# Performance work log

Hardware: AMD Instinct MI355X
Metric: run time of the kernel (lower is better)

## Reference

```python
import jax, jax.numpy as jnp
import numpy as np

N_NODES = 50000
N_EDGES = 800000


def setup_inputs() -> dict:
    key = jax.random.key(0)
    ks = jax.random.split(key, 8)
    return {
        "x": jax.random.normal(ks[0], (N_NODES, 256), dtype=jnp.float32),
        "adj_vals": jax.random.uniform(ks[1], (N_EDGES,), dtype=jnp.float32),
        "rows": jax.random.randint(ks[2], (N_EDGES,), 0, N_NODES, dtype=jnp.int32),
        "cols": jax.random.randint(ks[3], (N_EDGES,), 0, N_NODES, dtype=jnp.int32),
        "W1": jax.random.normal(ks[4], (256, 256), dtype=jnp.float32) * (1.0 / np.sqrt(256)),
        "b1": jnp.zeros((256,), dtype=jnp.float32),
        "W2": jax.random.normal(ks[5], (256, 256), dtype=jnp.float32) * (1.0 / np.sqrt(256)),
        "b2": jnp.zeros((256,), dtype=jnp.float32),
        "W3": jax.random.normal(ks[6], (256, 128), dtype=jnp.float32) * (1.0 / np.sqrt(256)),
        "b3": jnp.zeros((128,), dtype=jnp.float32),
    }


def reference(x, adj_vals, rows, cols, W1, b1, W2, b2, W3, b3):
    n = x.shape[0]

    def spmm(h):
        # sparse adjacency matmul: out[r] += val * h[c] over all edges (r, c)
        return jax.ops.segment_sum(adj_vals[:, None] * h[cols], rows, num_segments=n)

    # GCNLayer: adj @ (x @ W) + b ; ReLU between layers (dropout p=0 => identity)
    h = jax.nn.relu(spmm(x @ W1) + b1)
    h = jax.nn.relu(spmm(h @ W2) + b2)
    return spmm(h @ W3) + b3
```

## Files before the change

kernel.cpp:

```cpp
#include <hip/hip_runtime.h>
#include <hip/hip_bf16.h>


#define N_NODES 50000
#define N_EDGES 800000
#define KDIM 256
#define REP 8
#define NC (N_NODES * REP)
#define NB2 ((NC + 1023) / 1024)
#define NC_PAD (NB2 * 1024)

typedef __attribute__((ext_vector_type(8))) short short8;
typedef __attribute__((ext_vector_type(4))) float f32x4;

__device__ __forceinline__ ushort f2bf(float f) {
    union { float f; unsigned u; } x; x.f = f;
    unsigned r = x.u + 0x7fffu + ((x.u >> 16) & 1u);
    return (ushort)(r >> 16);
}
__device__ __forceinline__ float bf2f(ushort u) {
    union { unsigned u; float f; } x; x.u = ((unsigned)u) << 16;
    return x.f;
}

__global__ __launch_bounds__(256) void transpose_all_kernel(
        const float* __restrict__ W1, const float* __restrict__ W2,
        const float* __restrict__ W3, ushort* __restrict__ Wt1,
        ushort* __restrict__ Wt2, ushort* __restrict__ Wt3) {
    int id = blockIdx.x * blockDim.x + threadIdx.x;
    if (id < 65536) {
        int n = id >> 8, k = id & 255;
        Wt1[n * 256 + k] = f2bf(W1[k * 256 + n]);
    } else if (id < 131072) {
        int i = id - 65536, n = i >> 8, k = i & 255;
        Wt2[n * 256 + k] = f2bf(W2[k * 256 + n]);
    } else if (id < 163840) {
        int i = id - 131072, n = i >> 8, k = i & 255;
        Wt3[n * 256 + k] = f2bf(W3[k * 128 + n]);
    }
}


template <bool AFP32>
__device__ __forceinline__ void gemm_body(
        const void* __restrict__ Ain, const ushort* __restrict__ Wt,
        ushort* __restrict__ C, int M, int N, int bx, int by) {
    __shared__ ushort Ws[2048 * 8];

    int t = threadIdx.x;
    int lane = t & 63;
    int w = t >> 6;
    int row0 = bx * 128, col0 = by * 128;
    int wm = (w & 1) * 64, wn = (w >> 1) * 64;
    int q = lane >> 4, mi = lane & 15;

    const ushort* Ab = (const ushort*)Ain;
    const float*  Af = (const float*)Ain;

    f32x4 acc[4][4];
    #pragma unroll
    for (int i = 0; i < 4; i++)
        #pragma unroll
        for (int j = 0; j < 4; j++) acc[i][j] = (f32x4)0.f;

    for (int half = 0; half < 2; half++) {
        int kbase = half * 128;
        if (half) __syncthreads();
        #pragma unroll
        for (int i = 0; i < 8; i++) {
            int s = i * 256 + t;
            int scol = ((s >> 8) << 4) | (s & 15);
            int sk   = kbase + ((s >> 6) & 3) * 32 + ((s >> 4) & 3) * 8;
            *(short8*)&Ws[s * 8] =
                *(const short8*)&Wt[(size_t)(col0 + scol) * KDIM + sk];
        }
        __syncthreads();

        #pragma unroll
        for (int kb = 0; kb < 4; kb++) {
            int k0 = kbase + kb * 32;
            short8 af[4], bfr[4];
            #pragma unroll
            for (int mt = 0; mt < 4; mt++) {
                int ga = row0 + wm + mt * 16 + mi;
                if (ga >= M) ga = M - 1;
                if (AFP32) {
                    float4 f0 = *(const float4*)&Af[(size_t)ga * KDIM + k0 + q * 8];
                    float4 f1 = *(const float4*)&Af[(size_t)ga * KDIM + k0 + q * 8 + 4];
                    af[mt][0] = (short)f2bf(f0.x); af[mt][1] = (short)f2bf(f0.y);
                    af[mt][2] = (short)f2bf(f0.z); af[mt][3] = (short)f2bf(f0.w);
                    af[mt][4] = (short)f2bf(f1.x); af[mt][5] = (short)f2bf(f1.y);
                    af[mt][6] = (short)f2bf(f1.z); af[mt][7] = (short)f2bf(f1.w);
                } else {
                    af[mt] = *(const short8*)&Ab[(size_t)ga * KDIM + k0 + q * 8];
                }
            }
            #pragma unroll
            for (int nt = 0; nt < 4; nt++) {
                int g = (wn >> 4) + nt;
                bfr[nt] = *(const short8*)&Ws[((g * 4 + kb) * 64 + lane) * 8];
            }
            #pragma unroll
            for (int mt = 0; mt < 4; mt++)
                #pragma unroll
                for (int nt = 0; nt < 4; nt++)
                    acc[mt][nt] = __builtin_amdgcn_mfma_f32_16x16x32_bf16(
                        af[mt], bfr[nt], acc[mt][nt], 0, 0, 0);
        }
    }

    #pragma unroll
    for (int mt = 0; mt < 4; mt++) {
        #pragma unroll
        for (int r = 0; r < 4; r++) {
            int grow = row0 + wm + mt * 16 + q * 4 + r;
            if (grow < M) {
                #pragma unroll
                for (int nt = 0; nt < 4; nt++) {
                    int gcol = col0 + wn + nt * 16 + mi;
                    C[grow * N + gcol] = f2bf(acc[mt][nt][r]);
                }
            }
        }
    }
}

#define GB1 782

__global__ __launch_bounds__(256) void gemm1_hist_kernel(
        const float* __restrict__ x, const ushort* __restrict__ Wt1,
        ushort* __restrict__ C, const int* __restrict__ rows,
        int* __restrict__ counts) {
    int b = blockIdx.x;
    if (b < GB1) {
        gemm_body<true>(x, Wt1, C, N_NODES, 256, b % 391, b / 391);
    } else {
        int e = (b - GB1) * 256 + threadIdx.x;
        if (e < N_EDGES) {
            int r = rows[e];
            atomicAdd(&counts[(r << 3) | (e & 7)], 1);
        }
    }
}

template <bool AFP32>
__global__ __launch_bounds__(256) void gemm_bf16_kernel(
        const void* __restrict__ Ain, const ushort* __restrict__ Wt,
        ushort* __restrict__ C, int M, int N) {
    gemm_body<AFP32>(Ain, Wt, C, M, N, blockIdx.x, blockIdx.y);
}


__global__ __launch_bounds__(256) void scan_sums(const int* __restrict__ counts,
                                                 int* __restrict__ bsum) {
    __shared__ int ws[4];
    int b = blockIdx.x, t = threadIdx.x, lane = t & 63, wv = t >> 6;
    int4 v = *(const int4*)&counts[b * 1024 + t * 4];
    int s = v.x + v.y + v.z + v.w;
    #pragma unroll
    for (int off = 32; off >= 1; off >>= 1) s += __shfl_down(s, off, 64);
    if (lane == 0) ws[wv] = s;
    __syncthreads();
    if (t == 0) bsum[b] = ws[0] + ws[1] + ws[2] + ws[3];
}

__global__ __launch_bounds__(512) void scan_block(const int* __restrict__ bsum,
                                                  int* __restrict__ boff,
                                                  int* __restrict__ rp8, int nb) {
    __shared__ int ws[8];
    int t = threadIdx.x, lane = t & 63, wv = t >> 6;
    int v = (t < nb) ? bsum[t] : 0;
    int incl = v;
    #pragma unroll
    for (int off = 1; off < 64; off <<= 1) {
        int u = __shfl_up(incl, off, 64);
        if (lane >= off) incl += u;
    }
    if (lane == 63) ws[wv] = incl;
    __syncthreads();
    int wo = 0;
    #pragma unroll
    for (int j = 0; j < 7; j++) wo += (j < wv) ? ws[j] : 0;
    if (t < nb) boff[t] = wo + incl - v;
    if (t == 511) rp8[NC] = wo + incl;
}

__global__ __launch_bounds__(256) void scan_apply(int* __restrict__ counts,
                                                  const int* __restrict__ boff,
                                                  int* __restrict__ rp8) {
    __shared__ int ws[4];
    int b = blockIdx.x, t = threadIdx.x, lane = t & 63, wv = t >> 6;
    int i = b * 1024 + t * 4;
    int4 v = *(const int4*)&counts[i];
    int s0 = v.x, s01 = s0 + v.y, s012 = s01 + v.z, tsum = s012 + v.w;
    int incl = tsum;
    #pragma unroll
    for (int off = 1; off < 64; off <<= 1) {
        int u = __shfl_up(incl, off, 64);
        if (lane >= off) incl += u;
    }
    if (lane == 63) ws[wv] = incl;
    __syncthreads();
    int woff = 0;
    #pragma unroll
    for (int j = 0; j < 3; j++) woff += (j < wv) ? ws[j] : 0;
    int base = boff[b] + woff + incl - tsum;
    if (i < NC)     rp8[i]     = base;
    if (i + 1 < NC) rp8[i + 1] = base + s0;
    if (i + 2 < NC) rp8[i + 2] = base + s01;
    if (i + 3 < NC) rp8[i + 3] = base + s012;
    *(int4*)&counts[i] = make_int4(0, 0, 0, 0);
}

__global__ void scatter_kernel(const int* __restrict__ rows, const int* __restrict__ cols,
                               const float* __restrict__ vals, const int* __restrict__ rp8,
                               int* __restrict__ counts, int2* __restrict__ cv) {
    int e = blockIdx.x * blockDim.x + threadIdx.x;
    if (e < N_EDGES) {
        int idx = (rows[e] << 3) | (e & 7);
        int pos = rp8[idx] + atomicAdd(&counts[idx], 1);
        cv[pos] = make_int2(cols[e], __float_as_int(vals[e]));
    }
}


template <int F, bool RELU, bool OUT_BF16>
__global__ __launch_bounds__(256) void spmm_kernel(
        const ushort* __restrict__ H, const int* __restrict__ rp8,
        const int2* __restrict__ cv, const float* __restrict__ bias,
        void* __restrict__ out, int nrows) {
    constexpr int FL = F / 8;
    constexpr int EP = 64 / FL;
    constexpr int STEP = EP * 4;
    int wave = threadIdx.x >> 6, lane = threadIdx.x & 63;
    int r = blockIdx.x * 4 + wave;
    if (r >= nrows) return;
    int fl = lane % FL, ep = lane / FL;
    const ushort* Hl = H + fl * 8;

    float acc[8];
    #pragma unroll
    for (int j = 0; j < 8; j++) acc[j] = 0.f;

    int start = rp8[r * REP], end = rp8[r * REP + REP];
    for (int base = start; base < end; base += STEP) {
        int e0 = base + ep * 4;
        int2 m0 = cv[e0], m1 = cv[e0 + 1], m2 = cv[e0 + 2], m3 = cv[e0 + 3];
        int   c0 = (e0     < end) ? m0.x : 0;
        int   c1 = (e0 + 1 < end) ? m1.x : 0;
        int   c2 = (e0 + 2 < end) ? m2.x : 0;
        int   c3 = (e0 + 3 < end) ? m3.x : 0;
        float v0 = (e0     < end) ? __int_as_float(m0.y) : 0.f;
        float v1 = (e0 + 1 < end) ? __int_as_float(m1.y) : 0.f;
        float v2 = (e0 + 2 < end) ? __int_as_float(m2.y) : 0.f;
        float v3 = (e0 + 3 < end) ? __int_as_float(m3.y) : 0.f;
        short8 h0 = *(const short8*)&Hl[(size_t)c0 * F];
        short8 h1 = *(const short8*)&Hl[(size_t)c1 * F];
        short8 h2 = *(const short8*)&Hl[(size_t)c2 * F];
        short8 h3 = *(const short8*)&Hl[(size_t)c3 * F];
        #pragma unroll
        for (int j = 0; j < 8; j++)
            acc[j] += v0 * bf2f((ushort)h0[j]) + v1 * bf2f((ushort)h1[j])
                    + v2 * bf2f((ushort)h2[j]) + v3 * bf2f((ushort)h3[j]);
    }

    #pragma unroll
    for (int off = FL; off < 64; off <<= 1)
        #pragma unroll
        for (int j = 0; j < 8; j++) acc[j] += __shfl_down(acc[j], off, 64);

    if (ep == 0) {
        #pragma unroll
        for (int j = 0; j < 8; j++) {
            float o = acc[j] + bias[fl * 8 + j];
            if (RELU) o = fmaxf(o, 0.f);
            acc[j] = o;
        }
        if (OUT_BF16) {
            short8 ob;
            #pragma unroll
            for (int j = 0; j < 8; j++) ob[j] = (short)f2bf(acc[j]);
            *(short8*)((ushort*)out + (size_t)r * F + fl * 8) = ob;
        } else {
            float* of = (float*)out + (size_t)r * F + fl * 8;
            *(float4*)&of[0] = make_float4(acc[0], acc[1], acc[2], acc[3]);
            *(float4*)&of[4] = make_float4(acc[4], acc[5], acc[6], acc[7]);
        }
    }
}


extern "C" void kernel_launch(void* const* d_in, const int* in_sizes, int n_in,
                              void* d_out, int out_size, void* d_ws, size_t ws_size,
                              hipStream_t stream) {
    const float* x    = (const float*)d_in[0];
    const float* av   = (const float*)d_in[1];
    const int*   rows = (const int*)d_in[2];
    const int*   cols = (const int*)d_in[3];
    const float* W1   = (const float*)d_in[4];
    const float* b1   = (const float*)d_in[5];
    const float* W2   = (const float*)d_in[6];
    const float* b2   = (const float*)d_in[7];
    const float* W3   = (const float*)d_in[8];
    const float* b3   = (const float*)d_in[9];
    float* out = (float*)d_out;

    const int N = N_NODES, E = N_EDGES;

    char* p = (char*)d_ws;
    auto carve = [&](size_t bytes) {
        void* q = (void*)p;
        p += (bytes + 255) & ~(size_t)255;
        return q;
    };
    ushort* bufG = (ushort*)carve((size_t)N * 256 * 2);
    ushort* bufH = (ushort*)carve((size_t)N * 256 * 2);
    ushort* Wt1  = (ushort*)carve((size_t)256 * 256 * 2);
    ushort* Wt2  = (ushort*)carve((size_t)256 * 256 * 2);
    ushort* Wt3  = (ushort*)carve((size_t)128 * 256 * 2);
    int*    rp8    = (int*)carve((size_t)(NC + 1) * 4);
    int*    counts = (int*)carve((size_t)NC_PAD * 4);
    int*    bsum   = (int*)carve((size_t)NB2 * 4);
    int*    boff   = (int*)carve((size_t)NB2 * 4);
    int2*   cv     = (int2*)carve((size_t)(E + 16) * 8);

    hipMemsetAsync(counts, 0, (size_t)NC_PAD * 4, stream);
    transpose_all_kernel<<<(163840 + 255) / 256, 256, 0, stream>>>(W1, W2, W3, Wt1, Wt2, Wt3);

    gemm1_hist_kernel<<<GB1 + (E + 255) / 256, 256, 0, stream>>>(x, Wt1, bufG, rows, counts);

    scan_sums<<<NB2, 256, 0, stream>>>(counts, bsum);
    scan_block<<<1, 512, 0, stream>>>(bsum, boff, rp8, NB2);
    scan_apply<<<NB2, 256, 0, stream>>>(counts, boff, rp8);
    scatter_kernel<<<(E + 255) / 256, 256, 0, stream>>>(rows, cols, av, rp8, counts, cv);

    int spmm_blocks = (N + 3) / 4;
    spmm_kernel<256, true, true><<<spmm_blocks, 256, 0, stream>>>(bufG, rp8, cv, b1, bufH, N);
    gemm_bf16_kernel<false><<<dim3(391, 2), 256, 0, stream>>>(bufH, Wt2, bufG, N, 256);
    spmm_kernel<256, true, true><<<spmm_blocks, 256, 0, stream>>>(bufG, rp8, cv, b2, bufH, N);
    gemm_bf16_kernel<false><<<dim3(391, 1), 256, 0, stream>>>(bufH, Wt3, bufG, N, 128);
    spmm_kernel<128, false, false><<<spmm_blocks, 256, 0, stream>>>(bufG, rp8, cv, b3, out, N);
}
```

Before: 394.9 us.

## Double-buffer GEMM A/B tiles via async global-to-LDS loads and vectorize C stores

Restructures the dense GEMM body into an 8-step K loop with BK=32. A and B tiles are staged into double-buffered LDS using global_load_lds, so loads for the next step overlap MFMA work on the current one. A is now also read through LDS instead of directly from global memory. The output tile is staged through LDS and written back as 16-byte vector stores rather than scattered 2-byte stores. This raises LDS use (up to 48KB for the fp32 path) and adds one barrier per K step, which may reduce occupancy.

```diff
diff --git a/kernel.cpp b/kernel.cpp
--- a/kernel.cpp
+++ b/kernel.cpp
@@ -5,6 +5,7 @@
 #define N_NODES 50000
 #define N_EDGES 800000
 #define KDIM 256
+#define BK 32
 #define REP 8
 #define NC (N_NODES * REP)
 #define NB2 ((NC + 1023) / 1024)
@@ -21,6 +22,12 @@
 __device__ __forceinline__ float bf2f(ushort u) {
     union { unsigned u; float f; } x; x.u = ((unsigned)u) << 16;
     return x.f;
+}
+
+__device__ __forceinline__ void gld_lds16(const void* g, void* l) {
+    __builtin_amdgcn_global_load_lds(
+        (const __attribute__((address_space(1))) void*)g,
+        (__attribute__((address_space(3))) void*)l, 16, 0, 0);
 }
 
 __global__ __launch_bounds__(256) void transpose_all_kernel(
@@ -45,17 +52,60 @@
 __device__ __forceinline__ void gemm_body(
         const void* __restrict__ Ain, const ushort* __restrict__ Wt,
         ushort* __restrict__ C, int M, int N, int bx, int by) {
-    __shared__ ushort Ws[2048 * 8];
+    __shared__ char smem[AFP32 ? 49152 : 32768];
+    const int ABYTES = AFP32 ? 16384 : 8192;
 
     int t = threadIdx.x;
     int lane = t & 63;
     int w = t >> 6;
+    int wbase = w * 64;
     int row0 = bx * 128, col0 = by * 128;
-    int wm = (w & 1) * 64, wn = (w >> 1) * 64;
+    int wm2 = w & 1, wn2 = w >> 1;
+    int wm = wm2 * 64, wn = wn2 * 64;
     int q = lane >> 4, mi = lane & 15;
 
-    const ushort* Ab = (const ushort*)Ain;
+    char* Ab0 = smem;
+    char* Ab1 = smem + ABYTES;
+    char* Bb0 = smem + 2 * ABYTES;
+    char* Bb1 = smem + 2 * ABYTES + 8192;
+
     const float*  Af = (const float*)Ain;
+    const ushort* Au = (const ushort*)Ain;
+
+    auto stageA = [&](char* dst, int k0) {
+        if (AFP32) {
+            #pragma unroll
+            for (int i = 0; i < 4; i++) {
+                int D = i * 256 + t;
+                int h = D >> 9, s = D & 511;
+                int f = s >> 6, lp = s & 63;
+                int row = row0 + (f >> 2) * 64 + (f & 3) * 16 + (lp & 15);
+                if (row >= M) row = M - 1;
+                const float* g = Af + (size_t)row * KDIM + k0 + (lp >> 4) * 8 + h * 4;
+                gld_lds16(g, dst + (i * 256 + wbase) * 16);
+            }
+        } else {
+            #pragma unroll
+            for (int i = 0; i < 2; i++) {
+                int D = i * 256 + t;
+                int f = D >> 6, lp = D & 63;
+                int row = row0 + (f >> 2) * 64 + (f & 3) * 16 + (lp & 15);
+                if (row >= M) row = M - 1;
+                const ushort* g = Au + (size_t)row * KDIM + k0 + (lp >> 4) * 8;
+                gld_lds16(g, dst + (i * 256 + wbase) * 16);
+            }
+        }
+    };
+    auto stageB = [&](char* dst, int k0) {
+        #pragma unroll
+        for (int i = 0; i < 2; i++) {
+            int D = i * 256 + t;
+            int f = D >> 6, lp = D & 63;
+            int col = col0 + (f >> 2) * 64 + (f & 3) * 16 + (lp & 15);
+            const ushort* g = Wt + (size_t)col * KDIM + k0 + (lp >> 4) * 8;
+            gld_lds16(g, dst + (i * 256 + wbase) * 16);
+        }
+    };
 
     f32x4 acc[4][4];
     #pragma unroll
@@ -63,65 +113,69 @@
         #pragma unroll
         for (int j = 0; j < 4; j++) acc[i][j] = (f32x4)0.f;
 
-    for (int half = 0; half < 2; half++) {
-        int kbase = half * 128;
-        if (half) __syncthreads();
-        #pragma unroll
-        for (int i = 0; i < 8; i++) {
-            int s = i * 256 + t;
-            int scol = ((s >> 8) << 4) | (s & 15);
-            int sk   = kbase + ((s >> 6) & 3) * 32 + ((s >> 4) & 3) * 8;
-            *(short8*)&Ws[s * 8] =
-                *(const short8*)&Wt[(size_t)(col0 + scol) * KDIM + sk];
-        }
+    stageA(Ab0, 0);
+    stageB(Bb0, 0);
+    __syncthreads();
+
+    #pragma unroll
+    for (int kt = 0; kt < 8; kt++) {
+        char* Acur = (kt & 1) ? Ab1 : Ab0;
+        char* Bcur = (kt & 1) ? Bb1 : Bb0;
+        if (kt < 7) {
+            stageA((kt & 1) ? Ab0 : Ab1, (kt + 1) * BK);
+            stageB((kt & 1) ? Bb0 : Bb1, (kt + 1) * BK);
+        }
+
+        short8 af[4], bfr[4];
+        if (AFP32) {
+            const float* As = (const float*)Acur;
+            #pragma unroll
+            for (int mt = 0; mt < 4; mt++) {
+                int gA = (wm2 * 4 + mt) * 64 + lane;
+                f32x4 lo = *(const f32x4*)(As + gA * 4);
+                f32x4 hi = *(const f32x4*)(As + 2048 + gA * 4);
+                af[mt][0] = (short)f2bf(lo[0]); af[mt][1] = (short)f2bf(lo[1]);
+                af[mt][2] = (short)f2bf(lo[2]); af[mt][3] = (short)f2bf(lo[3]);
+                af[mt][4] = (short)f2bf(hi[0]); af[mt][5] = (short)f2bf(hi[1]);
+                af[mt][6] = (short)f2bf(hi[2]); af[mt][7] = (short)f2bf(hi[3]);
+            }
+        } else {
+            #pragma unroll
+            for (int mt = 0; mt < 4; mt++)
+                af[mt] = *(const short8*)(Acur + ((wm2 * 4 + mt) * 64 + lane) * 16);
+        }
+        #pragma unroll
+        for (int nt = 0; nt < 4; nt++)
+            bfr[nt] = *(const short8*)(Bcur + ((wn2 * 4 + nt) * 64 + lane) * 16);
+
+        #pragma unroll
+        for (int mt = 0; mt < 4; mt++)
+            #pragma unroll
+            for (int nt = 0; nt < 4; nt++)
+                acc[mt][nt] = __builtin_amdgcn_mfma_f32_16x16x32_bf16(
+                    af[mt], bfr[nt], acc[mt][nt], 0, 0, 0);
+
         __syncthreads();
-
-        #pragma unroll
-        for (int kb = 0; kb < 4; kb++) {
-            int k0 = kbase + kb * 32;
-            short8 af[4], bfr[4];
-            #pragma unroll
-            for (int mt = 0; mt < 4; mt++) {
-                int ga = row0 + wm + mt * 16 + mi;
-                if (ga >= M) ga = M - 1;
-                if (AFP32) {
-                    float4 f0 = *(const float4*)&Af[(size_t)ga * KDIM + k0 + q * 8];
-                    float4 f1 = *(const float4*)&Af[(size_t)ga * KDIM + k0 + q * 8 + 4];
-                    af[mt][0] = (short)f2bf(f0.x); af[mt][1] = (short)f2bf(f0.y);
-                    af[mt][2] = (short)f2bf(f0.z); af[mt][3] = (short)f2bf(f0.w);
-                    af[mt][4] = (short)f2bf(f1.x); af[mt][5] = (short)f2bf(f1.y);
-                    af[mt][6] = (short)f2bf(f1.z); af[mt][7] = (short)f2bf(f1.w);
-                } else {
-                    af[mt] = *(const short8*)&Ab[(size_t)ga * KDIM + k0 + q * 8];
-                }
-            }
-            #pragma unroll
-            for (int nt = 0; nt < 4; nt++) {
-                int g = (wn >> 4) + nt;
-                bfr[nt] = *(const short8*)&Ws[((g * 4 + kb) * 64 + lane) * 8];
-            }
-            #pragma unroll
-            for (int mt = 0; mt < 4; mt++)
-                #pragma unroll
-                for (int nt = 0; nt < 4; nt++)
-                    acc[mt][nt] = __builtin_amdgcn_mfma_f32_16x16x32_bf16(
-                        af[mt], bfr[nt], acc[mt][nt], 0, 0, 0);
-        }
-    }
-
-    #pragma unroll
-    for (int mt = 0; mt < 4; mt++) {
-        #pragma unroll
-        for (int r = 0; r < 4; r++) {
-            int grow = row0 + wm + mt * 16 + q * 4 + r;
-            if (grow < M) {
-                #pragma unroll
-                for (int nt = 0; nt < 4; nt++) {
-                    int gcol = col0 + wn + nt * 16 + mi;
-                    C[grow * N + gcol] = f2bf(acc[mt][nt][r]);
-                }
-            }
-        }
+    }
+
+    ushort* Cs = (ushort*)smem;
+    #pragma unroll
+    for (int mt = 0; mt < 4; mt++)
+        #pragma unroll
+        for (int r = 0; r < 4; r++)
+            #pragma unroll
+            for (int nt = 0; nt < 4; nt++)
+                Cs[(wm + mt * 16 + q * 4 + r) * 128 + wn + nt * 16 + mi] =
+                    f2bf(acc[mt][nt][r]);
+    __syncthreads();
+    #pragma unroll
+    for (int i = 0; i < 8; i++) {
+        int idx = i * 256 + t;
+        int rr = idx >> 4, gc = idx & 15;
+        int grow = row0 + rr;
+        if (grow < M)
+            *(short8*)&C[(size_t)grow * N + col0 + gc * 8] =
+                *(const short8*)&Cs[rr * 128 + gc * 8];
     }
 }
 
```

Measured after the change: 371.8 us. 1.06x faster.
